# Kernel optimization log

Measured on AMD Instinct MI355X. Metric: run time of the kernel, lower is better.

Reference implementation:

```python
import jax, jax.numpy as jnp
import numpy as np

ALPHA = 0.01  # load_balancing_alpha


def setup_inputs() -> dict:
    key = jax.random.key(0)
    ks = jax.random.split(key, 5)
    b, l, d, inter, E = 4, 2048, 1024, 2816, 8
    scale_h = 1.0
    return {
        "h": jax.random.normal(ks[0], (b, l, d), dtype=jnp.float32),
        "gate_w": jax.random.normal(ks[1], (d, E), dtype=jnp.float32) * (1.0 / np.sqrt(d)),
        "wg": jax.random.normal(ks[2], (E, d, inter), dtype=jnp.float32) * (1.0 / np.sqrt(d)),
        "wu": jax.random.normal(ks[3], (E, d, inter), dtype=jnp.float32) * (1.0 / np.sqrt(d)),
        "wd": jax.random.normal(ks[4], (E, inter, d), dtype=jnp.float32) * (1.0 / np.sqrt(inter)),
        "top_k": 2,
    }


def reference(h, gate_w, wg, wu, wd, top_k):
    # h: (b, l, d); gate_w: (d, E); wg/wu: (E, d, inter); wd: (E, inter, d)
    E = wg.shape[0]
    logits = jnp.einsum("bld,de->ble", h, gate_w)          # (b, l, E)
    w, sel = jax.lax.top_k(logits, top_k)                   # (b, l, k)
    w = jax.nn.softmax(w.astype(jnp.float32), axis=-1).astype(h.dtype)
    # route_probs_all: scatter top-k weights into (b, l, E), accumulate
    route = jnp.sum(jax.nn.one_hot(sel, E, dtype=h.dtype) * w[..., None], axis=2)  # (b, l, E)
    # dense dispatch: every expert processes all tokens, weighted combine
    results = jnp.zeros_like(h)
    for e in range(E):  # small fixed expert count
        g = h @ wg[e]                                        # (b, l, inter)
        act = jax.nn.silu(g) * (h @ wu[e])
        results = results + route[..., e:e + 1] * (act @ wd[e])
    # dropout with p=0.0 is identity
    p_i = route.mean(axis=(0, 1))                            # (E,)
    lb_loss = ALPHA * jnp.sum(p_i * p_i)
    return results, lb_loss, route
```

## Files before the change

kernel.cpp:

```cpp
#include <hip/hip_runtime.h>
#include <hip/hip_bf16.h>
#include <cstdio>

typedef short s16x8 __attribute__((ext_vector_type(8)));
typedef unsigned short u16x8 __attribute__((ext_vector_type(8)));
typedef float f32x4 __attribute__((ext_vector_type(4)));

#define B_TOK 8192
#define DDIM 1024
#define INTER 2816
#define NEXP 8
#define CAP_TILES 136
#define CAP_SLOTS (CAP_TILES * 128)

__device__ __forceinline__ unsigned short f2bf(float f) {
    unsigned int u = __float_as_uint(f);
    unsigned int r = u + 0x7fffu + ((u >> 16) & 1u);
    return (unsigned short)(r >> 16);
}

__device__ __forceinline__ float bf2f(unsigned short u) {
    unsigned int x = ((unsigned int)u) << 16;
    return __uint_as_float(x);
}

__device__ __forceinline__ void gload_lds16(const void* g, void* l) {
    __builtin_amdgcn_global_load_lds(
        (const __attribute__((address_space(1))) unsigned int*)g,
        (__attribute__((address_space(3))) unsigned int*)l, 16, 0, 0);
}

__global__ __launch_bounds__(256) void transpose_convert_v2(
    const float* __restrict__ src, unsigned short* __restrict__ dst,
    int K, int N) {
    __shared__ unsigned short tile[64][70];
    int e = blockIdx.z;
    src += (size_t)e * K * N;
    dst += (size_t)e * K * N;
    int n0 = blockIdx.x * 64, k0 = blockIdx.y * 64;
    int t = threadIdx.x;
    int lr = t >> 4;
    int lc = (t & 15) * 4;
#pragma unroll
    for (int p = 0; p < 4; ++p) {
        int kl = p * 16 + lr;
        float4 v = *(const float4*)(src + (size_t)(k0 + kl) * N + n0 + lc);
        tile[kl][lc + 0] = f2bf(v.x);
        tile[kl][lc + 1] = f2bf(v.y);
        tile[kl][lc + 2] = f2bf(v.z);
        tile[kl][lc + 3] = f2bf(v.w);
    }
    __syncthreads();
    int sn = t >> 3;
    int sk = (t & 7) * 8;
#pragma unroll
    for (int p = 0; p < 2; ++p) {
        int nl = p * 32 + sn;
        u16x8 o;
#pragma unroll
        for (int j = 0; j < 8; ++j) o[j] = tile[sk + j][nl];
        *(u16x8*)(dst + (size_t)(n0 + nl) * K + k0 + sk) = o;
    }
}

__global__ __launch_bounds__(256) void gating_kernel(
    const float* __restrict__ h,
    const float* __restrict__ gw,
    float* __restrict__ route,
    int* __restrict__ sel01,
    float2* __restrict__ wpair,
    int* __restrict__ counts,
    float* __restrict__ sums,
    unsigned short* __restrict__ hb) {
    __shared__ int lcnt[8];
    __shared__ float lsum[8];
    const int tid = threadIdx.x;
    if (tid < 8) { lcnt[tid] = 0; lsum[tid] = 0.f; }
    __syncthreads();
    const int wid = tid >> 6, lane = tid & 63;

    for (int t0 = 0; t0 < B_TOK; t0 += 1024) {
        int t = t0 + blockIdx.x * 4 + wid;
        const float* hp = h + (size_t)t * DDIM + lane * 16;
        float4 hv[4];
#pragma unroll
        for (int p = 0; p < 4; ++p) hv[p] = ((const float4*)hp)[p];

        u16x8 o0, o1;
        o0[0] = f2bf(hv[0].x); o0[1] = f2bf(hv[0].y); o0[2] = f2bf(hv[0].z); o0[3] = f2bf(hv[0].w);
        o0[4] = f2bf(hv[1].x); o0[5] = f2bf(hv[1].y); o0[6] = f2bf(hv[1].z); o0[7] = f2bf(hv[1].w);
        o1[0] = f2bf(hv[2].x); o1[1] = f2bf(hv[2].y); o1[2] = f2bf(hv[2].z); o1[3] = f2bf(hv[2].w);
        o1[4] = f2bf(hv[3].x); o1[5] = f2bf(hv[3].y); o1[6] = f2bf(hv[3].z); o1[7] = f2bf(hv[3].w);
        unsigned short* hbp = hb + (size_t)t * DDIM + lane * 16;
        *(u16x8*)hbp = o0;
        *(u16x8*)(hbp + 8) = o1;

        const float4* gp4 = (const float4*)(gw + (size_t)lane * 16 * NEXP);
        float s[8] = {0, 0, 0, 0, 0, 0, 0, 0};
#pragma unroll
        for (int p = 0; p < 4; ++p) {
#pragma unroll
            for (int q = 0; q < 4; ++q) {
                int kk = p * 4 + q;
                float hvk = (q == 0) ? hv[p].x : (q == 1) ? hv[p].y : (q == 2) ? hv[p].z : hv[p].w;
                float4 a = gp4[kk * 2], b = gp4[kk * 2 + 1];
                s[0] += hvk * a.x; s[1] += hvk * a.y; s[2] += hvk * a.z; s[3] += hvk * a.w;
                s[4] += hvk * b.x; s[5] += hvk * b.y; s[6] += hvk * b.z; s[7] += hvk * b.w;
            }
        }
#pragma unroll
        for (int off = 32; off > 0; off >>= 1) {
#pragma unroll
            for (int e = 0; e < 8; ++e) s[e] += __shfl_down(s[e], off);
        }
        if (lane == 0) {
            float m0 = -1e30f; int i0 = 0;
#pragma unroll
            for (int e = 0; e < 8; ++e) if (s[e] > m0) { m0 = s[e]; i0 = e; }
            float m1 = -1e30f; int i1 = -1;
#pragma unroll
            for (int e = 0; e < 8; ++e) if (e != i0 && s[e] > m1) { m1 = s[e]; i1 = e; }
            float d = __expf(m1 - m0);
            float w0 = 1.f / (1.f + d);
            float w1 = d * w0;
#pragma unroll
            for (int e = 0; e < 8; ++e)
                route[(size_t)t * 8 + e] = (e == i0) ? w0 : ((e == i1) ? w1 : 0.f);
            sel01[t] = i0 | (i1 << 8);
            wpair[t] = make_float2(w0, w1);
            atomicAdd(&lcnt[i0], 1);
            atomicAdd(&lcnt[i1], 1);
            atomicAdd(&lsum[i0], w0);
            atomicAdd(&lsum[i1], w1);
        }
    }
    __syncthreads();
    if (tid < 8) {
        atomicAdd(&counts[tid], lcnt[tid]);
        atomicAdd(&sums[tid], lsum[tid]);
    }
}

__global__ void setup_kernel(const int* __restrict__ counts,
                             const float* __restrict__ sums,
                             int* __restrict__ aoff,
                             int* __restrict__ tile_e,
                             int* __restrict__ tile_s0,
                             float* __restrict__ lb) {
    __shared__ int s_aoff[8], s_t0[9];
    if (threadIdx.x == 0) {
        int acc_slot = 0, acc_tile = 0;
        for (int e = 0; e < 8; ++e) {
            s_aoff[e] = acc_slot;
            s_t0[e] = acc_tile;
            int nt = (counts[e] + 127) >> 7;
            acc_slot += nt << 7;
            acc_tile += nt;
        }
        s_t0[8] = acc_tile;
        for (int e = 0; e < 8; ++e) aoff[e] = s_aoff[e];
        float acc = 0.f;
        for (int e = 0; e < 8; ++e) {
            float p = sums[e] / (float)B_TOK;
            acc += p * p;
        }
        lb[0] = 0.01f * acc;
    }
    __syncthreads();
    int t = threadIdx.x;
    if (t < CAP_TILES) {
        int e = -1, s0 = 0;
        for (int x = 0; x < 8; ++x)
            if (t >= s_t0[x] && t < s_t0[x + 1]) { e = x; s0 = s_aoff[x] + ((t - s_t0[x]) << 7); }
        tile_e[t] = e;
        tile_s0[t] = s0;
    }
}

__global__ __launch_bounds__(256) void fill_kernel(
    const int* __restrict__ sel01,
    const int* __restrict__ aoff,
    int* __restrict__ rank,
    int* __restrict__ idx,
    int2* __restrict__ tslot) {
    __shared__ int lcnt[8], lbase[8];
    const int tid = threadIdx.x;
    if (tid < 8) lcnt[tid] = 0;
    __syncthreads();
    int t = blockIdx.x * 256 + tid;
    int s = sel01[t];
    int e0 = s & 0xff, e1 = (s >> 8) & 0xff;
    int lr0 = atomicAdd(&lcnt[e0], 1);
    int lr1 = atomicAdd(&lcnt[e1], 1);
    __syncthreads();
    if (tid < 8) lbase[tid] = atomicAdd(&rank[tid], lcnt[tid]);
    __syncthreads();
    int sl0 = aoff[e0] + lbase[e0] + lr0;
    int sl1 = aoff[e1] + lbase[e1] + lr1;
    idx[sl0] = t;
    idx[sl1] = t;
    tslot[t] = make_int2(sl0, sl1);
}

__global__ __launch_bounds__(512, 2) void gemm1_sparse(
    const unsigned short* __restrict__ A,
    const unsigned short* __restrict__ Bg,
    const unsigned short* __restrict__ Bu,
    const int* __restrict__ tile_e,
    const int* __restrict__ tile_s0,
    const int* __restrict__ idx,
    unsigned short* __restrict__ act) {
    int e = tile_e[blockIdx.x];
    if (e < 0) return;
    const int slot0 = tile_s0[blockIdx.x];
    Bg += (size_t)e * DDIM * INTER;
    Bu += (size_t)e * DDIM * INTER;

    __shared__ unsigned short sA[2][128 * 32];
    __shared__ unsigned short sG[2][256 * 32];
    __shared__ unsigned short sU[2][256 * 32];
    const int tid = threadIdx.x, w = tid >> 6, lane = tid & 63;
    const int wr = w >> 2, wc = w & 3;
    const int colBase = blockIdx.y * 256;

    f32x4 accG[4][4], accU[4][4];
#pragma unroll
    for (int i = 0; i < 4; ++i)
#pragma unroll
        for (int j = 0; j < 4; ++j) { accG[i][j] = (f32x4)(0.f); accU[i][j] = (f32x4)(0.f); }

    const int srow = tid >> 2;
    const int skoff = (tid & 3) * 8;
    const size_t gA0 = (size_t)idx[slot0 + srow] * DDIM + skoff;
    const size_t gB0 = (size_t)(colBase + srow) * DDIM + skoff;
    const size_t gB1 = (size_t)(colBase + 128 + srow) * DDIM + skoff;

    const int rA = (lane & 15) * 32 + (lane >> 4) * 8;

    for (int k0 = 0; k0 < DDIM; k0 += 64) {
#pragma unroll
        for (int kk = 0; kk < 2; ++kk) {
            int k = k0 + kk * 32;
            gload_lds16(A + gA0 + k, sA[kk] + w * 512);
            gload_lds16(Bg + gB0 + k, sG[kk] + w * 512);
            gload_lds16(Bg + gB1 + k, sG[kk] + 4096 + w * 512);
            gload_lds16(Bu + gB0 + k, sU[kk] + w * 512);
            gload_lds16(Bu + gB1 + k, sU[kk] + 4096 + w * 512);
        }
        asm volatile("s_waitcnt vmcnt(0)" ::: "memory");
        __syncthreads();

#pragma unroll
        for (int kk = 0; kk < 2; ++kk) {
            s16x8 a[4], bg[4], bu[4];
#pragma unroll
            for (int mf = 0; mf < 4; ++mf)
                a[mf] = *(const s16x8*)&sA[kk][(wr * 64 + mf * 16) * 32 + rA];
#pragma unroll
            for (int nf = 0; nf < 4; ++nf) {
                bg[nf] = *(const s16x8*)&sG[kk][(wc * 64 + nf * 16) * 32 + rA];
                bu[nf] = *(const s16x8*)&sU[kk][(wc * 64 + nf * 16) * 32 + rA];
            }
#pragma unroll
            for (int mf = 0; mf < 4; ++mf)
#pragma unroll
                for (int nf = 0; nf < 4; ++nf) {
                    accG[mf][nf] = __builtin_amdgcn_mfma_f32_16x16x32_bf16(a[mf], bg[nf], accG[mf][nf], 0, 0, 0);
                    accU[mf][nf] = __builtin_amdgcn_mfma_f32_16x16x32_bf16(a[mf], bu[nf], accU[mf][nf], 0, 0, 0);
                }
        }
        __syncthreads();
    }

#pragma unroll
    for (int mf = 0; mf < 4; ++mf)
#pragma unroll
        for (int nf = 0; nf < 4; ++nf)
#pragma unroll
            for (int j = 0; j < 4; ++j) {
                int r = slot0 + wr * 64 + mf * 16 + (lane >> 4) * 4 + j;
                int c = colBase + wc * 64 + nf * 16 + (lane & 15);
                float g = accG[mf][nf][j], u = accU[mf][nf][j];
                float sg = 1.f / (1.f + __expf(-g));
                act[(size_t)r * INTER + c] = f2bf(g * sg * u);
            }
}

__global__ __launch_bounds__(256, 3) void gemm2_sparse_v4(
    const unsigned short* __restrict__ A,
    const unsigned short* __restrict__ Bd,
    const int* __restrict__ tile_e,
    const int* __restrict__ tile_s0,
    unsigned short* __restrict__ y) {
    int e = tile_e[blockIdx.x];
    if (e < 0) return;
    const int slot0 = tile_s0[blockIdx.x];
    const int colBase = blockIdx.y * 128;
    Bd += (size_t)e * DDIM * INTER;

    __shared__ unsigned short sA[2][128 * 32];
    __shared__ unsigned short sB[2][128 * 32];
    const int tid = threadIdx.x, wid = tid >> 6, lane = tid & 63;
    const int wr = wid >> 1, wc = wid & 1;

    f32x4 acc[4][4];
#pragma unroll
    for (int i = 0; i < 4; ++i)
#pragma unroll
        for (int j = 0; j < 4; ++j) acc[i][j] = (f32x4)(0.f);

    const int c0 = wid, c1 = wid + 4;
    const int srow = lane >> 2;
    const int skoff = (lane & 3) * 8;
    const int rA = (lane & 15) * 32 + (lane >> 4) * 8;

    const size_t gA0 = (size_t)(slot0 + c0 * 16 + srow) * INTER + skoff;
    const size_t gA1 = (size_t)(slot0 + c1 * 16 + srow) * INTER + skoff;
    const size_t gB0 = (size_t)(colBase + c0 * 16 + srow) * INTER + skoff;
    const size_t gB1 = (size_t)(colBase + c1 * 16 + srow) * INTER + skoff;

    for (int k0 = 0; k0 < INTER; k0 += 64) {
#pragma unroll
        for (int kk = 0; kk < 2; ++kk) {
            int k = k0 + kk * 32;
            gload_lds16(A + gA0 + k, sA[kk] + c0 * 512);
            gload_lds16(A + gA1 + k, sA[kk] + c1 * 512);
            gload_lds16(Bd + gB0 + k, sB[kk] + c0 * 512);
            gload_lds16(Bd + gB1 + k, sB[kk] + c1 * 512);
        }
        asm volatile("s_waitcnt vmcnt(0)" ::: "memory");
        __syncthreads();

#pragma unroll
        for (int kk = 0; kk < 2; ++kk) {
            s16x8 a[4], b[4];
#pragma unroll
            for (int mf = 0; mf < 4; ++mf)
                a[mf] = *(const s16x8*)&sA[kk][(wr * 64 + mf * 16) * 32 + rA];
#pragma unroll
            for (int nf = 0; nf < 4; ++nf)
                b[nf] = *(const s16x8*)&sB[kk][(wc * 64 + nf * 16) * 32 + rA];
#pragma unroll
            for (int mf = 0; mf < 4; ++mf)
#pragma unroll
                for (int nf = 0; nf < 4; ++nf)
                    acc[mf][nf] = __builtin_amdgcn_mfma_f32_16x16x32_bf16(a[mf], b[nf], acc[mf][nf], 0, 0, 0);
        }
        __syncthreads();
    }

#pragma unroll
    for (int mf = 0; mf < 4; ++mf)
#pragma unroll
        for (int j = 0; j < 4; ++j) {
            int slot = slot0 + wr * 64 + mf * 16 + (lane >> 4) * 4 + j;
#pragma unroll
            for (int nf = 0; nf < 4; ++nf) {
                int c = colBase + wc * 64 + nf * 16 + (lane & 15);
                y[(size_t)slot * DDIM + c] = f2bf(acc[mf][nf][j]);
            }
        }
}

__global__ __launch_bounds__(256) void combine_kernel(
    const unsigned short* __restrict__ y,
    const int2* __restrict__ tslot,
    const float2* __restrict__ wpair,
    float* __restrict__ out) {
    int gid = blockIdx.x * 256 + threadIdx.x;
    int tok = gid >> 7;
    int c8 = (gid & 127) * 8;
    int2 ts = tslot[tok];
    float2 w = wpair[tok];
    u16x8 a = *(const u16x8*)(y + (size_t)ts.x * DDIM + c8);
    u16x8 b = *(const u16x8*)(y + (size_t)ts.y * DDIM + c8);
    float4 r0, r1;
    r0.x = w.x * bf2f(a[0]) + w.y * bf2f(b[0]);
    r0.y = w.x * bf2f(a[1]) + w.y * bf2f(b[1]);
    r0.z = w.x * bf2f(a[2]) + w.y * bf2f(b[2]);
    r0.w = w.x * bf2f(a[3]) + w.y * bf2f(b[3]);
    r1.x = w.x * bf2f(a[4]) + w.y * bf2f(b[4]);
    r1.y = w.x * bf2f(a[5]) + w.y * bf2f(b[5]);
    r1.z = w.x * bf2f(a[6]) + w.y * bf2f(b[6]);
    r1.w = w.x * bf2f(a[7]) + w.y * bf2f(b[7]);
    float* op = out + (size_t)tok * DDIM + c8;
    *(float4*)op = r0;
    *(float4*)(op + 4) = r1;
}


extern "C" void kernel_launch(void* const* d_in, const int* in_sizes, int n_in,
                              void* d_out, int out_size, void* d_ws, size_t ws_size,
                              hipStream_t stream) {
    const float* h = (const float*)d_in[0];
    const float* gate_w = (const float*)d_in[1];
    const float* wg = (const float*)d_in[2];
    const float* wu = (const float*)d_in[3];
    const float* wd = (const float*)d_in[4];

    float* out = (float*)d_out;
    float* lb = out + (size_t)B_TOK * DDIM;
    float* route = lb + 1;

    const size_t SZ_META = 1 << 20;
    const size_t SZ_HB = (size_t)B_TOK * DDIM * 2;
    const size_t SZ_W = (size_t)NEXP * DDIM * INTER * 2;
    const size_t SZ_ACT = (size_t)CAP_SLOTS * INTER * 2;
    const size_t NEED = SZ_META + SZ_HB + 2 * SZ_W + SZ_ACT;
    if (ws_size < NEED) {
        fprintf(stderr, "kernel_launch: ws too small: %zu < %zu\n", ws_size, NEED);
        return;
    }
    char* ws = (char*)d_ws;
    int* counts = (int*)(ws + 0);
    int* rank = (int*)(ws + 32);
    int* aoff = (int*)(ws + 64);
    float* sums = (float*)(ws + 96);
    int* tile_e = (int*)(ws + 128);
    int* tile_s0 = (int*)(ws + 1024);
    int* sel01 = (int*)(ws + 2048);
    float2* wpair = (float2*)(ws + 34816);
    int* idx = (int*)(ws + 100352);
    int2* tslot = (int2*)(ws + 262144);

    unsigned short* hb = (unsigned short*)(ws + SZ_META);
    unsigned short* wgT = (unsigned short*)(ws + SZ_META + SZ_HB);
    unsigned short* wuT = (unsigned short*)(ws + SZ_META + SZ_HB + SZ_W);
    unsigned short* act = (unsigned short*)(ws + SZ_META + SZ_HB + 2 * SZ_W);
    unsigned short* wdT = wgT;
    unsigned short* y = wuT;

    hipMemsetAsync(ws, 0, SZ_META, stream);

    transpose_convert_v2<<<dim3(INTER / 64, DDIM / 64, NEXP), 256, 0, stream>>>(wg, wgT, DDIM, INTER);
    transpose_convert_v2<<<dim3(INTER / 64, DDIM / 64, NEXP), 256, 0, stream>>>(wu, wuT, DDIM, INTER);

    gating_kernel<<<256, 256, 0, stream>>>(h, gate_w, route, sel01, wpair, counts, sums, hb);
    setup_kernel<<<1, 256, 0, stream>>>(counts, sums, aoff, tile_e, tile_s0, lb);
    fill_kernel<<<B_TOK / 256, 256, 0, stream>>>(sel01, aoff, rank, idx, tslot);

    gemm1_sparse<<<dim3(CAP_TILES, INTER / 256), 512, 0, stream>>>(
        hb, wgT, wuT, tile_e, tile_s0, idx, act);

    transpose_convert_v2<<<dim3(DDIM / 64, INTER / 64, NEXP), 256, 0, stream>>>(wd, wdT, INTER, DDIM);

    gemm2_sparse_v4<<<dim3(CAP_TILES, DDIM / 128), 256, 0, stream>>>(
        act, wdT, tile_e, tile_s0, y);

    combine_kernel<<<(B_TOK * 128) / 256, 256, 0, stream>>>(y, tslot, wpair, out);
}
```

Baseline: 578.7 us.

## Rewrite gate/up GEMM as 8-phase software-pipelined kernel with swizzled LDS

Replaces the gemm1 main loop, which loaded everything and then waited on vmcnt(0), with an 8-phase schedule over a double-buffered 64-wide K tile. Global-to-LDS loads for the next tile are interleaved with MFMA phases using partial vmcnt waits, barriers and setprio. The LDS layout is XOR-swizzled to reduce bank conflicts. It also raises gemm2's launch-bounds occupancy hint from 3 to 4, and brings a much larger LDS footprint (160 KB) and fragile hand-tuned wait counts.

After: 500.4 us. 1.16x faster.

```diff
diff --git a/kernel.cpp b/kernel.cpp
--- a/kernel.cpp
+++ b/kernel.cpp
@@ -202,7 +202,7 @@
     tslot[t] = make_int2(sl0, sl1);
 }
 
-__global__ __launch_bounds__(512, 2) void gemm1_sparse(
+__global__ __launch_bounds__(512, 2) void gemm1_8ph(
     const unsigned short* __restrict__ A,
     const unsigned short* __restrict__ Bg,
     const unsigned short* __restrict__ Bu,
@@ -213,63 +213,97 @@
     int e = tile_e[blockIdx.x];
     if (e < 0) return;
     const int slot0 = tile_s0[blockIdx.x];
-    Bg += (size_t)e * DDIM * INTER;
-    Bu += (size_t)e * DDIM * INTER;
-
-    __shared__ unsigned short sA[2][128 * 32];
-    __shared__ unsigned short sG[2][256 * 32];
-    __shared__ unsigned short sU[2][256 * 32];
-    const int tid = threadIdx.x, w = tid >> 6, lane = tid & 63;
+    const int colBase = blockIdx.y * 256;
+    const unsigned short* Gp = Bg + (size_t)e * DDIM * INTER;
+    const unsigned short* Up = Bu + (size_t)e * DDIM * INTER;
+
+    __shared__ unsigned short lds[81920];
+
+    const int t = threadIdx.x;
+    const int w = t >> 6, lane = t & 63;
     const int wr = w >> 2, wc = w & 3;
-    const int colBase = blockIdx.y * 256;
+    const int l15 = lane & 15;
+    const int kb8 = (lane >> 4) * 8;
+    const int t8 = t * 8;
+    const int rowIdx = t >> 3;
+    const int kus = ((t & 7) * 8) ^ (((t >> 3) & 7) << 3);
+
+    const unsigned short* Ab0 = A + (size_t)idx[slot0 + rowIdx] * DDIM + kus;
+    const unsigned short* Ab1 = A + (size_t)idx[slot0 + 64 + rowIdx] * DDIM + kus;
+    const unsigned int gbase = (unsigned int)(colBase + rowIdx) * DDIM + kus;
 
     f32x4 accG[4][4], accU[4][4];
 #pragma unroll
     for (int i = 0; i < 4; ++i)
 #pragma unroll
-        for (int j = 0; j < 4; ++j) { accG[i][j] = (f32x4)(0.f); accU[i][j] = (f32x4)(0.f); }
-
-    const int srow = tid >> 2;
-    const int skoff = (tid & 3) * 8;
-    const size_t gA0 = (size_t)idx[slot0 + srow] * DDIM + skoff;
-    const size_t gB0 = (size_t)(colBase + srow) * DDIM + skoff;
-    const size_t gB1 = (size_t)(colBase + 128 + srow) * DDIM + skoff;
-
-    const int rA = (lane & 15) * 32 + (lane >> 4) * 8;
-
-    for (int k0 = 0; k0 < DDIM; k0 += 64) {
-#pragma unroll
-        for (int kk = 0; kk < 2; ++kk) {
-            int k = k0 + kk * 32;
-            gload_lds16(A + gA0 + k, sA[kk] + w * 512);
-            gload_lds16(Bg + gB0 + k, sG[kk] + w * 512);
-            gload_lds16(Bg + gB1 + k, sG[kk] + 4096 + w * 512);
-            gload_lds16(Bu + gB0 + k, sU[kk] + w * 512);
-            gload_lds16(Bu + gB1 + k, sU[kk] + 4096 + w * 512);
-        }
-        asm volatile("s_waitcnt vmcnt(0)" ::: "memory");
-        __syncthreads();
-
-#pragma unroll
-        for (int kk = 0; kk < 2; ++kk) {
-            s16x8 a[4], bg[4], bu[4];
-#pragma unroll
-            for (int mf = 0; mf < 4; ++mf)
-                a[mf] = *(const s16x8*)&sA[kk][(wr * 64 + mf * 16) * 32 + rA];
-#pragma unroll
-            for (int nf = 0; nf < 4; ++nf) {
-                bg[nf] = *(const s16x8*)&sG[kk][(wc * 64 + nf * 16) * 32 + rA];
-                bu[nf] = *(const s16x8*)&sU[kk][(wc * 64 + nf * 16) * 32 + rA];
-            }
-#pragma unroll
-            for (int mf = 0; mf < 4; ++mf)
-#pragma unroll
-                for (int nf = 0; nf < 4; ++nf) {
-                    accG[mf][nf] = __builtin_amdgcn_mfma_f32_16x16x32_bf16(a[mf], bg[nf], accG[mf][nf], 0, 0, 0);
-                    accU[mf][nf] = __builtin_amdgcn_mfma_f32_16x16x32_bf16(a[mf], bu[nf], accU[mf][nf], 0, 0, 0);
-                }
-        }
-        __syncthreads();
+        for (int jq = 0; jq < 4; ++jq) { accG[i][jq] = (f32x4)(0.f); accU[i][jq] = (f32x4)(0.f); }
+
+#define STA(s, kt) { \
+    gload_lds16(Ab0 + (kt) * 64, (void*)(lds + (s) * 40960 + t8)); \
+    gload_lds16(Ab1 + (kt) * 64, (void*)(lds + (s) * 40960 + 4096 + t8)); }
+#define STG(s, hh, kt) { \
+    gload_lds16(Gp + gbase + (2 * (hh)) * 65536 + (kt) * 64,     (void*)(lds + (s) * 40960 + 8192 + (2 * (hh)) * 4096 + t8)); \
+    gload_lds16(Gp + gbase + (2 * (hh) + 1) * 65536 + (kt) * 64, (void*)(lds + (s) * 40960 + 8192 + (2 * (hh) + 1) * 4096 + t8)); }
+#define STU(s, hh, kt) { \
+    gload_lds16(Up + gbase + (2 * (hh)) * 65536 + (kt) * 64,     (void*)(lds + (s) * 40960 + 24576 + (2 * (hh)) * 4096 + t8)); \
+    gload_lds16(Up + gbase + (2 * (hh) + 1) * 65536 + (kt) * 64, (void*)(lds + (s) * 40960 + 24576 + (2 * (hh) + 1) * 4096 + t8)); }
+#define DSA(s, kk) { _Pragma("unroll") for (int mf = 0; mf < 4; ++mf) { \
+    int lr = wr * 64 + mf * 16 + l15; \
+    a[mf] = *(const s16x8*)&lds[(s) * 40960 + lr * 64 + (((kk) * 32 + kb8) ^ ((lr & 7) << 3))]; } }
+#define DSB(dst, s, off, kk) { _Pragma("unroll") for (int nf = 0; nf < 4; ++nf) { \
+    int rr = wc * 64 + nf * 16 + l15; \
+    dst[nf] = *(const s16x8*)&lds[(s) * 40960 + (off) + rr * 64 + (((kk) * 32 + kb8) ^ ((rr & 7) << 3))]; } }
+#define MM(ACC, B) { _Pragma("unroll") for (int mf = 0; mf < 4; ++mf) \
+    _Pragma("unroll") for (int nf = 0; nf < 4; ++nf) \
+        ACC[mf][nf] = __builtin_amdgcn_mfma_f32_16x16x32_bf16(a[mf], B[nf], ACC[mf][nf], 0, 0, 0); }
+#define PH_TAIL(ACC, B) \
+    __builtin_amdgcn_s_barrier(); \
+    asm volatile("s_waitcnt lgkmcnt(0)" ::: "memory"); \
+    __builtin_amdgcn_sched_barrier(0); \
+    __builtin_amdgcn_s_setprio(1); \
+    MM(ACC, B); \
+    __builtin_amdgcn_s_setprio(0); \
+    __builtin_amdgcn_sched_barrier(0); \
+    __builtin_amdgcn_s_barrier();
+
+    STA(0, 0); STG(0, 0, 0); STG(0, 1, 0); STU(0, 0, 0); STU(0, 1, 0);
+    STA(1, 1); STG(1, 0, 1);
+    asm volatile("s_waitcnt vmcnt(8)" ::: "memory");
+    __builtin_amdgcn_s_barrier();
+
+    s16x8 a[4], bg[4], bu[4];
+#pragma unroll 1
+    for (int j = 0; j < 8; ++j) {
+        const bool nl = (j < 7);
+        const int t1 = 2 * j + 1, t2 = 2 * j + 2, t3 = 2 * j + 3;
+        DSA(0, 0); DSB(bg, 0, 8192, 0);
+        STG(1, 1, t1); STU(1, 0, t1);
+        asm volatile("s_waitcnt vmcnt(8)" ::: "memory");
+        PH_TAIL(accG, bg);
+        DSB(bu, 0, 24576, 0);
+        STU(1, 1, t1);
+        PH_TAIL(accU, bu);
+        DSA(0, 1); DSB(bg, 0, 8192, 1);
+        PH_TAIL(accG, bg);
+        DSB(bu, 0, 24576, 1);
+        if (nl) { STA(0, t2); STG(0, 0, t2); }
+        if (nl) { asm volatile("s_waitcnt vmcnt(6)" ::: "memory"); }
+        else    { asm volatile("s_waitcnt vmcnt(4)" ::: "memory"); }
+        PH_TAIL(accU, bu);
+        DSA(1, 0); DSB(bg, 1, 8192, 0);
+        if (nl) { STG(0, 1, t2); STU(0, 0, t2); }
+        if (nl) { asm volatile("s_waitcnt vmcnt(8)" ::: "memory"); }
+        else    { asm volatile("s_waitcnt vmcnt(0)" ::: "memory"); }
+        PH_TAIL(accG, bg);
+        DSB(bu, 1, 24576, 0);
+        if (nl) { STU(0, 1, t2); }
+        PH_TAIL(accU, bu);
+        DSA(1, 1); DSB(bg, 1, 8192, 1);
+        PH_TAIL(accG, bg);
+        DSB(bu, 1, 24576, 1);
+        if (nl) { STA(1, t3); STG(1, 0, t3); }
+        if (nl) { asm volatile("s_waitcnt vmcnt(6)" ::: "memory"); }
+        PH_TAIL(accU, bu);
     }
 
 #pragma unroll
@@ -277,16 +311,23 @@
 #pragma unroll
         for (int nf = 0; nf < 4; ++nf)
 #pragma unroll
-            for (int j = 0; j < 4; ++j) {
-                int r = slot0 + wr * 64 + mf * 16 + (lane >> 4) * 4 + j;
-                int c = colBase + wc * 64 + nf * 16 + (lane & 15);
-                float g = accG[mf][nf][j], u = accU[mf][nf][j];
+            for (int jq = 0; jq < 4; ++jq) {
+                int r = slot0 + wr * 64 + mf * 16 + (lane >> 4) * 4 + jq;
+                int c = colBase + wc * 64 + nf * 16 + l15;
+                float g = accG[mf][nf][jq], u = accU[mf][nf][jq];
                 float sg = 1.f / (1.f + __expf(-g));
                 act[(size_t)r * INTER + c] = f2bf(g * sg * u);
             }
-}
-
-__global__ __launch_bounds__(256, 3) void gemm2_sparse_v4(
+#undef STA
+#undef STG
+#undef STU
+#undef DSA
+#undef DSB
+#undef MM
+#undef PH_TAIL
+}
+
+__global__ __launch_bounds__(256, 4) void gemm2_sparse_v4(
     const unsigned short* __restrict__ A,
     const unsigned short* __restrict__ Bd,
     const int* __restrict__ tile_e,
@@ -439,7 +480,7 @@
     setup_kernel<<<1, 256, 0, stream>>>(counts, sums, aoff, tile_e, tile_s0, lb);
     fill_kernel<<<B_TOK / 256, 256, 0, stream>>>(sel01, aoff, rank, idx, tslot);
 
-    gemm1_sparse<<<dim3(CAP_TILES, INTER / 256), 512, 0, stream>>>(
+    gemm1_8ph<<<dim3(CAP_TILES, INTER / 256), 512, 0, stream>>>(
         hb, wgT, wuT, tile_e, tile_s0, idx, act);
 
     transpose_convert_v2<<<dim3(DDIM / 64, INTER / 64, NEXP), 256, 0, stream>>>(wd, wdT, INTER, DDIM);
```
